# Kernel optimization log

Measured on AMD Instinct MI355X. Metric: run time of the kernel, lower is better.

## Reference

```python
import jax, jax.numpy as jnp
import numpy as np

D_MODEL = 1024
NHEAD = 16
D_K = D_MODEL // NHEAD
MAX_REL = 1024


def setup_inputs() -> dict:
    key = jax.random.key(0)
    ks = jax.random.split(key, 6)
    B, S = 4, 2048
    s = 1.0 / np.sqrt(D_MODEL)
    x = jax.random.normal(ks[0], (B, S, D_MODEL), dtype=jnp.float32)
    W_qkv = jax.random.normal(ks[1], (D_MODEL, 3 * D_MODEL), dtype=jnp.float32) * s
    b_qkv = jnp.zeros((3 * D_MODEL,), dtype=jnp.float32)
    W_out = jax.random.normal(ks[2], (D_MODEL, D_MODEL), dtype=jnp.float32) * s
    b_out = jnp.zeros((D_MODEL,), dtype=jnp.float32)
    # torch init is zeros; use small random so bias path is exercised
    rel_bias = jax.random.normal(ks[3], (2 * MAX_REL + 1, NHEAD), dtype=jnp.float32) * 0.02
    return {"x": x, "W_qkv": W_qkv, "b_qkv": b_qkv, "W_out": W_out,
            "b_out": b_out, "rel_bias": rel_bias}


def reference(x, W_qkv, b_qkv, W_out, b_out, rel_bias):
    B, S, D = x.shape
    qkv = x @ W_qkv + b_qkv                      # [B,S,3D]
    qkv = qkv.reshape(B, S, 3, NHEAD, D_K)
    q, k, v = qkv[:, :, 0], qkv[:, :, 1], qkv[:, :, 2]  # [B,S,H,dk]
    # scores: [B,H,S,S]
    scores = jnp.einsum('bihd,bjhd->bhij', q, k) / jnp.sqrt(jnp.float32(D_K))
    idxs = jnp.arange(S)
    rel = jnp.clip(idxs[:, None] - idxs[None, :] + MAX_REL, 0, 2 * MAX_REL)  # [S,S]
    bias = rel_bias[rel]                         # [S,S,H]
    scores = scores + jnp.transpose(bias, (2, 0, 1))[None]  # broadcast over batch
    attn = jax.nn.softmax(scores, axis=-1)       # dropout p=0 (eval)
    out = jnp.einsum('bhij,bjhd->bihd', attn, v).reshape(B, S, D)
    return out @ W_out + b_out
```

## Files before the change

kernel.cpp:

```cpp
#include <hip/hip_runtime.h>

#define S_LEN 2048
#define NHEADS 16
#define DK 64
#define DMODEL 1024
#define QSCALE 0.18033688011f

typedef float f32x4 __attribute__((ext_vector_type(4)));
typedef _Float16 f16x8 __attribute__((ext_vector_type(8)));
typedef _Float16 f16x4 __attribute__((ext_vector_type(4)));
typedef __fp16 h16x2 __attribute__((ext_vector_type(2)));

__device__ __forceinline__ unsigned short f2h_bits(float f) {
  _Float16 h = (_Float16)f;
  unsigned short u; __builtin_memcpy(&u, &h, 2); return u;
}

__device__ __forceinline__ f32x4 mfma16(f16x8 a, f16x8 b, f32x4 c) {
  return __builtin_amdgcn_mfma_f32_16x16x32_f16(a, b, c, 0, 0, 0);
}
__device__ __forceinline__ f32x4 mfma16k16(f16x4 a, f16x4 b, f32x4 c) {
  return __builtin_amdgcn_mfma_f32_16x16x16f16(a, b, c, 0, 0, 0);
}
__device__ __forceinline__ f16x8 frag_ld(const unsigned short* p) {
  return *(const f16x8*)p;
}

#define GLD_LDS(g, l)                                                          \
  __builtin_amdgcn_global_load_lds(                                            \
      (const __attribute__((address_space(1))) void*)(g),                      \
      (__attribute__((address_space(3))) void*)(l), 16, 0, 0)

__global__ void convert_f32_f16(const float* __restrict__ in,
                                unsigned short* __restrict__ out, int n4) {
  int i = blockIdx.x * blockDim.x + threadIdx.x;
  if (i < n4) {
    f32x4 v = *(const f32x4*)(in + (size_t)i * 4);
    unsigned short o[4];
#pragma unroll
    for (int j = 0; j < 4; j++) o[j] = f2h_bits(v[j]);
    *(uint2*)(out + (size_t)i * 4) = *(const uint2*)o;
  }
}

__global__ void transpose_f32_f16(const float* __restrict__ in,
                                  unsigned short* __restrict__ out, int R, int C) {
  __shared__ unsigned short tile[32][33];
  int bx = blockIdx.x * 32, by = blockIdx.y * 32;
  int tx = threadIdx.x, ty = threadIdx.y;
  for (int i = ty; i < 32; i += 8)
    tile[i][tx] = f2h_bits(in[(size_t)(by + i) * C + bx + tx]);
  __syncthreads();
  for (int i = ty; i < 32; i += 8)
    out[(size_t)(bx + i) * R + by + tx] = tile[tx][i];
}

__launch_bounds__(256)
__global__ void gemm_bt(const unsigned short* __restrict__ A,
                        const unsigned short* __restrict__ Bt,
                        int M, int N, int K, int mode,
                        const float* __restrict__ bias,
                        float* __restrict__ out0,
                        unsigned short* __restrict__ q_o,
                        unsigned short* __restrict__ k_o,
                        unsigned short* __restrict__ v_o) {
  __shared__ __attribute__((aligned(16))) unsigned short As[128 * 32];
  __shared__ __attribute__((aligned(16))) unsigned short Bs[128 * 32];
  const int tid = threadIdx.x;
  const int w = tid >> 6, lane = tid & 63;
  const int wm = w >> 1, wn = w & 1;
  const int col = lane & 15, quad = lane >> 4;
  const int m0 = blockIdx.y * 128, n0 = blockIdx.x * 128;
  const f32x4 fzero = {0.f, 0.f, 0.f, 0.f};
  f32x4 acc[4][4];
#pragma unroll
  for (int i = 0; i < 4; i++)
#pragma unroll
    for (int j = 0; j < 4; j++) acc[i][j] = fzero;

  for (int k0 = 0; k0 < K; k0 += 32) {
    __syncthreads();
#pragma unroll
    for (int it = 0; it < 2; it++) {
      int c = it * 256 + tid;
      GLD_LDS(A + (size_t)(m0 + (c >> 2)) * K + k0 + (c & 3) * 8, &As[c * 8]);
      GLD_LDS(Bt + (size_t)(n0 + (c >> 2)) * K + k0 + (c & 3) * 8, &Bs[c * 8]);
    }
    __syncthreads();
    f16x8 af[4], bfr[4];
#pragma unroll
    for (int mi = 0; mi < 4; mi++)
      af[mi] = frag_ld(&As[(wm * 64 + mi * 16 + col) * 32 + quad * 8]);
#pragma unroll
    for (int ni = 0; ni < 4; ni++)
      bfr[ni] = frag_ld(&Bs[(wn * 64 + ni * 16 + col) * 32 + quad * 8]);
#pragma unroll
    for (int mi = 0; mi < 4; mi++)
#pragma unroll
      for (int ni = 0; ni < 4; ni++)
        acc[mi][ni] = mfma16(af[mi], bfr[ni], acc[mi][ni]);
  }

#pragma unroll
  for (int mi = 0; mi < 4; mi++) {
#pragma unroll
    for (int ni = 0; ni < 4; ni++) {
      int gm_b = m0 + wm * 64 + mi * 16 + quad * 4;
      int gn = n0 + wn * 64 + ni * 16 + col;
      float bv = bias[gn];
      if (mode == 1) {
#pragma unroll
        for (int r = 0; r < 4; r++)
          out0[(size_t)(gm_b + r) * N + gn] = acc[mi][ni][r] + bv;
      } else {
        int b = gm_b >> 11, s0 = gm_b & 2047;
        int t = gn >> 10, hd = gn & 1023;
        int h = hd >> 6, d = hd & 63;
        size_t bh = (size_t)(b * NHEADS + h);
        if (t == 2) {
          unsigned short o4[4];
#pragma unroll
          for (int r = 0; r < 4; r++) o4[r] = f2h_bits(acc[mi][ni][r] + bv);
          *(uint2*)&v_o[(bh * DK + d) * S_LEN + s0] = *(const uint2*)o4;
        } else {
          unsigned short* dst = (t == 0) ? q_o : k_o;
          float sc = (t == 0) ? QSCALE : 1.0f;
#pragma unroll
          for (int r = 0; r < 4; r++)
            dst[(bh * S_LEN + s0 + r) * DK + d] = f2h_bits((acc[mi][ni][r] + bv) * sc);
        }
      }
    }
  }
}

__launch_bounds__(256)
__global__ void attn_kernel(const unsigned short* __restrict__ Q,
                            const unsigned short* __restrict__ K,
                            const unsigned short* __restrict__ Vt,
                            const float* __restrict__ rel_bias,
                            unsigned short* __restrict__ ctx) {
  __shared__ __attribute__((aligned(16))) unsigned short Ks[2][64 * 64];
  __shared__ __attribute__((aligned(16))) unsigned short Vs[2][64 * 64];
  __shared__ float brev[4096];
  const int tid = threadIdx.x;
  const int w = tid >> 6, lane = tid & 63;
  const int col = lane & 15, quad = lane >> 4;
  const int c7 = col & 7;
  const int bid = blockIdx.x;
  const int xcd = bid & 7, slot = bid >> 3;
  const int bh = (slot >> 5) * 8 + xcd;
  const int qt = slot & 31;
  const int h = bh & (NHEADS - 1), b = bh >> 4;
  const unsigned short* qp = Q + (size_t)bh * S_LEN * DK;
  const unsigned short* kp = K + (size_t)bh * S_LEN * DK;
  const unsigned short* vp = Vt + (size_t)bh * DK * S_LEN;
  const f32x4 fzero = {0.f, 0.f, 0.f, 0.f};
  const f16x4 ones = {(_Float16)1.f, (_Float16)1.f, (_Float16)1.f, (_Float16)1.f};

#pragma unroll
  for (int it = 0; it < 16; it++) {
    int t = it * 256 + tid;
    int rel = 3072 - t;
    rel = rel < 0 ? 0 : (rel > 2048 ? 2048 : rel);
    brev[t] = rel_bias[rel * NHEADS + h] * 1.44269504089f;
  }

  const int row_base = qt * 64 + w * 16;
  f16x8 qa0 = frag_ld(qp + (size_t)(row_base + col) * DK + quad * 8);
  f16x8 qa1 = frag_ld(qp + (size_t)(row_base + col) * DK + 32 + quad * 8);

  const int tq = quad * 4 - (row_base + col) + 2048;

  f32x4 o[4];
  f32x4 lacc = fzero;
#pragma unroll
  for (int ni = 0; ni < 4; ni++) o[ni] = fzero;

  auto stage = [&](int bi, int jj) {
#pragma unroll
    for (int it = 0; it < 2; it++) {
      int c = it * 256 + tid;
      int row = c >> 3, gs = c & 7, g = gs ^ (row & 7);
      GLD_LDS(kp + (size_t)(jj + row) * DK + g * 8, &Ks[bi][c * 8]);
      GLD_LDS(vp + (size_t)row * S_LEN + jj + g * 8, &Vs[bi][c * 8]);
    }
  };

  stage(0, 0);

  for (int ck = 0; ck < S_LEN / 64; ck++) {
    const int j0 = ck * 64;
    const int cur = ck & 1;
    __syncthreads();
    if (ck < S_LEN / 64 - 1) stage(cur ^ 1, j0 + 64);

    const float* bp = &brev[j0 + tq];
    f32x4 sc4[4];
#pragma unroll
    for (int ni = 0; ni < 4; ni++) {
      f32x4 bias4;
#pragma unroll
      for (int r = 0; r < 4; r++) bias4[r] = bp[ni * 16 + r];
      f16x8 kb0 = frag_ld(&Ks[cur][(ni * 16 + col) * 64 + (quad ^ c7) * 8]);
      f16x8 kb1 = frag_ld(&Ks[cur][(ni * 16 + col) * 64 + ((quad | 4) ^ c7) * 8]);
      sc4[ni] = mfma16(kb1, qa1, mfma16(kb0, qa0, bias4));
    }
    f16x4 pa[4];
#pragma unroll
    for (int ni = 0; ni < 4; ni++) {
      float p0 = __builtin_amdgcn_exp2f(sc4[ni][0]);
      float p1 = __builtin_amdgcn_exp2f(sc4[ni][1]);
      float p2 = __builtin_amdgcn_exp2f(sc4[ni][2]);
      float p3 = __builtin_amdgcn_exp2f(sc4[ni][3]);
      h16x2 lo = __builtin_amdgcn_cvt_pkrtz(p0, p1);
      h16x2 hi = __builtin_amdgcn_cvt_pkrtz(p2, p3);
      f16x4 t;
      __builtin_memcpy(&t, &lo, 4);
      __builtin_memcpy(((char*)&t) + 4, &hi, 4);
      pa[ni] = t;
    }
#pragma unroll
    for (int ni_d = 0; ni_d < 4; ni_d++) {
#pragma unroll
      for (int ni_k = 0; ni_k < 4; ni_k++) {
        int g = ni_k * 2 + (quad >> 1);
        f16x4 vb = *(const f16x4*)&Vs[cur][(ni_d * 16 + col) * 64 + (g ^ c7) * 8 + (quad & 1) * 4];
        o[ni_d] = mfma16k16(pa[ni_k], vb, o[ni_d]);
      }
    }
#pragma unroll
    for (int ni_k = 0; ni_k < 4; ni_k++)
      lacc = mfma16k16(pa[ni_k], ones, lacc);
  }
  float inv_r[4];
#pragma unroll
  for (int r = 0; r < 4; r++) inv_r[r] = 1.0f / lacc[r];
#pragma unroll
  for (int r = 0; r < 4; r++) {
    int srow = row_base + quad * 4 + r;
#pragma unroll
    for (int ni = 0; ni < 4; ni++) {
      int d = ni * 16 + col;
      ctx[((size_t)b * S_LEN + srow) * DMODEL + h * DK + d] = f2h_bits(o[ni][r] * inv_r[r]);
    }
  }
}

extern "C" void kernel_launch(void* const* d_in, const int* in_sizes, int n_in,
                              void* d_out, int out_size, void* d_ws, size_t ws_size,
                              hipStream_t stream) {
  (void)in_sizes; (void)n_in; (void)out_size; (void)ws_size;
  const float* x        = (const float*)d_in[0];
  const float* W_qkv    = (const float*)d_in[1];
  const float* b_qkv    = (const float*)d_in[2];
  const float* W_out    = (const float*)d_in[3];
  const float* b_out    = (const float*)d_in[4];
  const float* rel_bias = (const float*)d_in[5];
  float* out = (float*)d_out;

  char* ws = (char*)d_ws;
  unsigned short* xh     = (unsigned short*)(ws + 0);
  unsigned short* ctxh   = (unsigned short*)(ws + 0);
  unsigned short* Wqkv_t = (unsigned short*)(ws + 16777216);
  unsigned short* Wout_t = (unsigned short*)(ws + 23068672);
  unsigned short* Qb     = (unsigned short*)(ws + 25165824);
  unsigned short* Kb     = (unsigned short*)(ws + 41943040);
  unsigned short* Vtb    = (unsigned short*)(ws + 58720256);

  convert_f32_f16<<<(8192 * 1024 / 4 + 255) / 256, 256, 0, stream>>>(x, xh, 8192 * 1024 / 4);
  transpose_f32_f16<<<dim3(3072 / 32, 1024 / 32), dim3(32, 8), 0, stream>>>(W_qkv, Wqkv_t, 1024, 3072);
  transpose_f32_f16<<<dim3(1024 / 32, 1024 / 32), dim3(32, 8), 0, stream>>>(W_out, Wout_t, 1024, 1024);
  gemm_bt<<<dim3(3072 / 128, 8192 / 128), 256, 0, stream>>>(
      xh, Wqkv_t, 8192, 3072, 1024, 0, b_qkv, nullptr, Qb, Kb, Vtb);
  attn_kernel<<<4 * NHEADS * (S_LEN / 64), 256, 0, stream>>>(Qb, Kb, Vtb, rel_bias, ctxh);
  gemm_bt<<<dim3(1024 / 128, 8192 / 128), 256, 0, stream>>>(
      ctxh, Wout_t, 8192, 1024, 1024, 1, b_out, out, nullptr, nullptr, nullptr);
}
```

Measured before the change: 342.0 us.

## Single-buffer K/V tiles and shrink bias table to per-tile window for occupancy

Drops the double-buffered K/V shared tiles in favor of a single buffer with load-then-sync each chunk, and shrinks the precomputed relative-bias table from 4096 to 2112 entries covering only the window needed by this query tile. Together these cut LDS per block substantially, aiming to fit more blocks per CU. The cost is losing the overlap of next-chunk loads with compute and adding a second barrier per iteration.

```diff
diff --git a/kernel.cpp b/kernel.cpp
--- a/kernel.cpp
+++ b/kernel.cpp
@@ -140,9 +140,9 @@
                             const unsigned short* __restrict__ Vt,
                             const float* __restrict__ rel_bias,
                             unsigned short* __restrict__ ctx) {
-  __shared__ __attribute__((aligned(16))) unsigned short Ks[2][64 * 64];
-  __shared__ __attribute__((aligned(16))) unsigned short Vs[2][64 * 64];
-  __shared__ float brev[4096];
+  __shared__ __attribute__((aligned(16))) unsigned short Ks[64 * 64];
+  __shared__ __attribute__((aligned(16))) unsigned short Vs[64 * 64];
+  __shared__ float brev[2112];
   const int tid = threadIdx.x;
   const int w = tid >> 6, lane = tid & 63;
   const int col = lane & 15, quad = lane >> 4;
@@ -158,52 +158,49 @@
   const f32x4 fzero = {0.f, 0.f, 0.f, 0.f};
   const f16x4 ones = {(_Float16)1.f, (_Float16)1.f, (_Float16)1.f, (_Float16)1.f};
 
-#pragma unroll
-  for (int it = 0; it < 16; it++) {
-    int t = it * 256 + tid;
-    int rel = 3072 - t;
-    rel = rel < 0 ? 0 : (rel > 2048 ? 2048 : rel);
-    brev[t] = rel_bias[rel * NHEADS + h] * 1.44269504089f;
+  const int tbase = 1985 - qt * 64;
+#pragma unroll
+  for (int it = 0; it < 9; it++) {
+    int idx = it * 256 + tid;
+    if (idx < 2112) {
+      int rel = 3072 - (tbase + idx);
+      rel = rel < 0 ? 0 : (rel > 2048 ? 2048 : rel);
+      brev[idx] = rel_bias[rel * NHEADS + h] * 1.44269504089f;
+    }
   }
 
   const int row_base = qt * 64 + w * 16;
   f16x8 qa0 = frag_ld(qp + (size_t)(row_base + col) * DK + quad * 8);
   f16x8 qa1 = frag_ld(qp + (size_t)(row_base + col) * DK + 32 + quad * 8);
 
-  const int tq = quad * 4 - (row_base + col) + 2048;
+  const int tql = quad * 4 - w * 16 - col + 63;
 
   f32x4 o[4];
   f32x4 lacc = fzero;
 #pragma unroll
   for (int ni = 0; ni < 4; ni++) o[ni] = fzero;
 
-  auto stage = [&](int bi, int jj) {
+  for (int ck = 0; ck < S_LEN / 64; ck++) {
+    const int j0 = ck * 64;
+    __syncthreads();
 #pragma unroll
     for (int it = 0; it < 2; it++) {
       int c = it * 256 + tid;
       int row = c >> 3, gs = c & 7, g = gs ^ (row & 7);
-      GLD_LDS(kp + (size_t)(jj + row) * DK + g * 8, &Ks[bi][c * 8]);
-      GLD_LDS(vp + (size_t)row * S_LEN + jj + g * 8, &Vs[bi][c * 8]);
-    }
-  };
-
-  stage(0, 0);
-
-  for (int ck = 0; ck < S_LEN / 64; ck++) {
-    const int j0 = ck * 64;
-    const int cur = ck & 1;
-    __syncthreads();
-    if (ck < S_LEN / 64 - 1) stage(cur ^ 1, j0 + 64);
-
-    const float* bp = &brev[j0 + tq];
+      GLD_LDS(kp + (size_t)(j0 + row) * DK + g * 8, &Ks[c * 8]);
+      GLD_LDS(vp + (size_t)row * S_LEN + j0 + g * 8, &Vs[c * 8]);
+    }
+    __syncthreads();
+
+    const float* bp = &brev[j0 + tql];
     f32x4 sc4[4];
 #pragma unroll
     for (int ni = 0; ni < 4; ni++) {
       f32x4 bias4;
 #pragma unroll
       for (int r = 0; r < 4; r++) bias4[r] = bp[ni * 16 + r];
-      f16x8 kb0 = frag_ld(&Ks[cur][(ni * 16 + col) * 64 + (quad ^ c7) * 8]);
-      f16x8 kb1 = frag_ld(&Ks[cur][(ni * 16 + col) * 64 + ((quad | 4) ^ c7) * 8]);
+      f16x8 kb0 = frag_ld(&Ks[(ni * 16 + col) * 64 + (quad ^ c7) * 8]);
+      f16x8 kb1 = frag_ld(&Ks[(ni * 16 + col) * 64 + ((quad | 4) ^ c7) * 8]);
       sc4[ni] = mfma16(kb1, qa1, mfma16(kb0, qa0, bias4));
     }
     f16x4 pa[4];
@@ -225,7 +222,7 @@
 #pragma unroll
       for (int ni_k = 0; ni_k < 4; ni_k++) {
         int g = ni_k * 2 + (quad >> 1);
-        f16x4 vb = *(const f16x4*)&Vs[cur][(ni_d * 16 + col) * 64 + (g ^ c7) * 8 + (quad & 1) * 4];
+        f16x4 vb = *(const f16x4*)&Vs[(ni_d * 16 + col) * 64 + (g ^ c7) * 8 + (quad & 1) * 4];
         o[ni_d] = mfma16k16(pa[ni_k], vb, o[ni_d]);
       }
     }
```

Measured after the change: 334.7 us. 2.1% less time.
